# Optimization experiments

Measured on AMD Instinct MI355X. Metric: run time of the kernel, lower is better.

The kernel has to match this reference:

```python
import jax, jax.numpy as jnp
import numpy as np

QMIN, QMAX = 0, 255        # 8-bit asymmetric activation quant bounds
GROUP_SIZE = 128

def setup_inputs() -> dict:
    key = jax.random.key(0)
    k1, k2, k3, k4, k5 = jax.random.split(key, 5)
    x = jax.random.normal(k1, (1, 2048, 4096), dtype=jnp.float32)
    qweight = jax.random.randint(k2, (4096, 32, 128), 0, 16, dtype=jnp.int32)  # uint4 codes
    w_scales = jax.random.uniform(k3, (4096, 32), dtype=jnp.float32, minval=0.001, maxval=0.02)
    w_zero_points = jax.random.randint(k4, (4096, 32), 0, 16, dtype=jnp.int32)
    bias = jax.random.normal(k5, (4096,), dtype=jnp.float32)
    return {"x": x, "qweight": qweight, "w_scales": w_scales,
            "w_zero_points": w_zero_points, "bias": bias}

def reference(x, qweight, w_scales, w_zero_points, bias):
    xf = x.astype(jnp.float32)
    # per-token (last-dim) asymmetric dynamic activation quantization
    xmin = jnp.min(xf, axis=-1, keepdims=True)
    xmax = jnp.max(xf, axis=-1, keepdims=True)
    x_scale = jnp.clip((xmax - xmin) / (QMAX - QMIN), 1e-5, None)
    x_zp = jnp.clip(jnp.round(-xmin / x_scale), QMIN, QMAX)
    q = jnp.clip(jnp.round(xf / x_scale) + x_zp, QMIN, QMAX)
    centered_x = (q - x_zp).reshape(*x.shape[:-1], -1, GROUP_SIZE)  # [B,S,G,C]
    # grouped weight dequant (zero-point centered)
    centered_w = qweight.astype(jnp.float32) - w_zero_points.astype(jnp.float32)[..., None]  # [O,G,C]
    acc = jnp.einsum('bsgc,ogc->bsog', centered_x, centered_w)  # [B,S,O,G]
    out = (acc * w_scales[None, None]).sum(axis=-1)  # apply per-group weight scales
    out = out * x_scale  # per-token activation scale
    out = out + bias
    return out
```

## Files before the change

### kernel.cpp

```cpp
#include <hip/hip_runtime.h>
#include <stdint.h>

#define M_DIM 2048
#define N_DIM 4096
#define K_DIM 4096
#define NGROUP 32
#define GSIZE 128

#define RQ_UP   (127.0f / 15.0f)
#define RQ_DOWN (15.0f / 127.0f)

#define BM 256
#define BN 128
#define KSLICE 64
#define NSLICE (K_DIM / KSLICE)
#define BSLOT (BN * KSLICE)

typedef __attribute__((ext_vector_type(4))) int int32x4_t;

static __device__ __forceinline__ void gl2lds16(const void* g, void* l) {
    auto gp = (const __attribute__((address_space(1))) unsigned int*)(uintptr_t)g;
    auto lp = (__attribute__((address_space(3))) unsigned int*)(uintptr_t)l;
    __builtin_amdgcn_global_load_lds(gp, lp, 16, 0, 0);
}

#define WAITVM_(N) asm volatile("s_waitcnt vmcnt(" #N ")" ::: "memory")
#define WAITVM(N) WAITVM_(N)
#define WAITLGKM_(N) asm volatile("s_waitcnt lgkmcnt(" #N ")" ::: "memory")
#define WAITLGKM(N) WAITLGKM_(N)
#define BARRIER() asm volatile("s_barrier" ::: "memory")

#define QUANT_BLOCKS M_DIM
#define DEQ_BLOCKS ((N_DIM * K_DIM) / 8 / 256)

__global__ __launch_bounds__(256) void prep_kernel(
        const float* __restrict__ x,
        const int* __restrict__ qw,
        const float* __restrict__ wsc,
        const int* __restrict__ wzp,
        char* __restrict__ A8,
        char* __restrict__ Bt8,
        float* __restrict__ xscale,
        float* __restrict__ xzpc,
        int* __restrict__ Sw)
{
    const int t = threadIdx.x;
    if (blockIdx.x < QUANT_BLOCKS) {
        const int s = blockIdx.x;
        const float* xrow = x + (size_t)s * K_DIM;

        float xv[16];
        float vmin = 1e38f, vmax = -1e38f;
#pragma unroll
        for (int p = 0; p < 4; ++p) {
            float4 v = *((const float4*)(xrow + p * 1024) + t);
            xv[p*4+0] = v.x; xv[p*4+1] = v.y; xv[p*4+2] = v.z; xv[p*4+3] = v.w;
            vmin = fminf(vmin, fminf(fminf(v.x, v.y), fminf(v.z, v.w)));
            vmax = fmaxf(vmax, fmaxf(fmaxf(v.x, v.y), fmaxf(v.z, v.w)));
        }
#pragma unroll
        for (int off = 32; off > 0; off >>= 1) {
            vmin = fminf(vmin, __shfl_xor(vmin, off));
            vmax = fmaxf(vmax, __shfl_xor(vmax, off));
        }
        __shared__ float smin[4], smax[4];
        const int wave = t >> 6;
        if ((t & 63) == 0) { smin[wave] = vmin; smax[wave] = vmax; }
        __syncthreads();
        vmin = fminf(fminf(smin[0], smin[1]), fminf(smin[2], smin[3]));
        vmax = fmaxf(fmaxf(smax[0], smax[1]), fmaxf(smax[2], smax[3]));

        float sc = (vmax - vmin) / 255.0f;
        sc = fmaxf(sc, 1e-5f);
        float zp = rintf(-vmin / sc);
        zp = fminf(fmaxf(zp, 0.0f), 255.0f);

#pragma unroll
        for (int p = 0; p < 4; ++p) {
            int b[4];
#pragma unroll
            for (int e = 0; e < 4; ++e) {
                float q = fminf(fmaxf(rintf(xv[p*4+e] / sc) + zp, 0.0f), 255.0f);
                b[e] = (int)q - 128;
            }
            unsigned pack = (b[0] & 0xff) | ((b[1] & 0xff) << 8) |
                            ((b[2] & 0xff) << 16) | ((b[3] & 0xff) << 24);
            *(unsigned*)(A8 + (size_t)s * K_DIM + p * 1024 + t * 4) = pack;
        }
        if (t == 0) { xscale[s] = sc; xzpc[s] = 128.0f - zp; }
    } else {
        const size_t base = ((size_t)(blockIdx.x - QUANT_BLOCKS) * 256 + t) * 8;
        const int n = (int)(base >> 12);
        const int g = (int)((base >> 7) & 31);
        const int zp = wzp[n * NGROUP + g];

        const int cl = t & 15;
        float2 wp = *(const float2*)(wsc + (size_t)n * NGROUP + cl * 2);
        float smx = fmaxf(wp.x, wp.y);
#pragma unroll
        for (int off = 1; off < 16; off <<= 1)
            smx = fmaxf(smx, __shfl_xor(smx, off));
        const float factor = wsc[n * NGROUP + g] * (RQ_UP / smx);

        int4 c0 = *(const int4*)(qw + base);
        int4 c1 = *(const int4*)(qw + base + 4);
        int w[8];
        w[0] = (int)rintf((float)(c0.x - zp) * factor);
        w[1] = (int)rintf((float)(c0.y - zp) * factor);
        w[2] = (int)rintf((float)(c0.z - zp) * factor);
        w[3] = (int)rintf((float)(c0.w - zp) * factor);
        w[4] = (int)rintf((float)(c1.x - zp) * factor);
        w[5] = (int)rintf((float)(c1.y - zp) * factor);
        w[6] = (int)rintf((float)(c1.z - zp) * factor);
        w[7] = (int)rintf((float)(c1.w - zp) * factor);
        uint2 pk;
        pk.x = (w[0] & 0xff) | ((w[1] & 0xff) << 8) | ((w[2] & 0xff) << 16) | ((w[3] & 0xff) << 24);
        pk.y = (w[4] & 0xff) | ((w[5] & 0xff) << 8) | ((w[6] & 0xff) << 16) | ((w[7] & 0xff) << 24);
        *(uint2*)(Bt8 + base) = pk;

        int s8 = w[0] + w[1] + w[2] + w[3] + w[4] + w[5] + w[6] + w[7];
#pragma unroll
        for (int off = 1; off < 16; off <<= 1) s8 += __shfl_xor(s8, off);
        if ((t & 15) == 0)
            Sw[n * NGROUP + g] = s8;
    }
}

__global__ __launch_bounds__(512, 1) void gemm_kernel(
        const char* __restrict__ A8,
        const char* __restrict__ Bt8,
        const float* __restrict__ xscale,
        const float* __restrict__ xzpc,
        const float* __restrict__ wsc,
        const int* __restrict__ Sw,
        const float* __restrict__ bias,
        float* __restrict__ out)
{
    __shared__ __align__(16) char Bs[4][BSLOT];
    __shared__ float fws_s[BN], wsf_s[BN];

    const int tid  = threadIdx.x;
    const int bn   = blockIdx.x;
    const int bm   = blockIdx.y;
    const int wave = tid >> 6;
    const int lane = tid & 63;
    const int wr   = wave >> 1;
    const int wcl  = wave & 1;
    const int lrow  = lane & 15;
    const int lquad = lane >> 4;

    if (tid < BN) {
        const int n = bn * BN + tid;
        const int4* s4 = (const int4*)(Sw + (size_t)n * NGROUP);
        int acc = 0;
#pragma unroll
        for (int p = 0; p < 8; ++p) { int4 v = s4[p]; acc += v.x + v.y + v.z + v.w; }
        const float4* w4 = (const float4*)(wsc + (size_t)n * NGROUP);
        float s = 0.f;
#pragma unroll
        for (int p = 0; p < 8; ++p) {
            float4 w = w4[p];
            s = fmaxf(s, fmaxf(fmaxf(w.x, w.y), fmaxf(w.z, w.w)));
        }
        const float fw = s * RQ_DOWN;
        fws_s[tid] = fw;
        wsf_s[tid] = fw * (float)acc;
    }
    asm volatile("s_waitcnt vmcnt(0) lgkmcnt(0)" ::: "memory");

    const char* Bb = Bt8 + (size_t)(bn * BN) * K_DIM;
    const int lsub = lane >> 2;
    const int csrc = (lane & 3) ^ ((lane >> 3) & 3);
    const char* gB0 = Bb + (size_t)(wave * 16 + lsub) * K_DIM + csrc * 16;
    const int lB0 = wave * 1024;

    const char* gA = A8 + (size_t)(bm * BM + wr * 64 + lrow) * K_DIM + lquad * 16;

    const int xq = (lquad ^ ((lrow >> 1) & 3)) * 16;
    int boff[4];
#pragma unroll
    for (int j = 0; j < 4; ++j)
        boff[j] = (wcl * 64 + j * 16 + lrow) * KSLICE + xq;

    int32x4_t iacc[4][4];
    const int32x4_t zi = {0, 0, 0, 0};
#pragma unroll
    for (int i = 0; i < 4; ++i)
#pragma unroll
        for (int j = 0; j < 4; ++j) iacc[i][j] = zi;

    int32x4_t aX[4], aY[4], bX[4], bY[4];

#define STAGEB(t) gl2lds16(gB0 + (size_t)(t) * KSLICE, &Bs[(t) & 3][0] + lB0)

#define LOADA(t, ar) {                                                \
        _Pragma("unroll")                                             \
        for (int i_ = 0; i_ < 4; ++i_)                                \
            ar[i_] = *(const int32x4_t*)(gA + (size_t)i_ * 16 * K_DIM \
                                            + (size_t)(t) * KSLICE);  \
    }

#define READB(t, br) {                                                \
        const char* Bp_ = &Bs[(t) & 3][0];                            \
        _Pragma("unroll")                                             \
        for (int j_ = 0; j_ < 4; ++j_)                                \
            br[j_] = *(const int32x4_t*)(Bp_ + boff[j_]);             \
    }

#define MFMAS(ar, br) {                                               \
        __builtin_amdgcn_s_setprio(1);                                \
        _Pragma("unroll")                                             \
        for (int i_ = 0; i_ < 4; ++i_)                                \
            _Pragma("unroll")                                         \
            for (int j_ = 0; j_ < 4; ++j_)                            \
                iacc[i_][j_] = __builtin_amdgcn_mfma_i32_16x16x64_i8( \
                    ar[i_], br[j_], iacc[i_][j_], 0, 0, 0);           \
        __builtin_amdgcn_s_setprio(0);                                \
    }

#define BODY(s, VMN, AC, AN, BC, BNX) {                               \
        if ((s) + 3 < NSLICE) STAGEB((s) + 3);                        \
        WAITVM(VMN);                                                  \
        BARRIER();                                                    \
        READB((s) + 1, BNX);                                          \
        WAITLGKM(4);                                                  \
        __builtin_amdgcn_sched_barrier(0);                            \
        MFMAS(AC, BC);                                                \
        if ((s) + 2 < NSLICE) LOADA((s) + 2, AC);                     \
    }

    STAGEB(0); LOADA(0, aX);
    STAGEB(1); LOADA(1, aY);
    STAGEB(2);
    WAITVM(10);
    BARRIER();
    READB(0, bX);

    for (int s = 0; s < NSLICE - 4; s += 2) {
        BODY(s,     6, aX, aY, bX, bY);
        BODY(s + 1, 6, aY, aX, bY, bX);
    }
    BODY(60, 6, aX, aY, bX, bY);
    BODY(61, 5, aY, aX, bY, bX);
    WAITVM(4);
    BARRIER();
    READB(63, bY);
    WAITLGKM(4);
    __builtin_amdgcn_sched_barrier(0);
    MFMAS(aX, bX);
    WAITVM(0);
    WAITLGKM(0);
    __builtin_amdgcn_sched_barrier(0);
    MFMAS(aY, bY);

    float fn[4], wf[4], bb[4];
    int ncol[4];
#pragma unroll
    for (int j = 0; j < 4; ++j) {
        const int ncl = wcl * 64 + j * 16 + lrow;
        ncol[j] = bn * BN + ncl;
        fn[j] = fws_s[ncl];
        wf[j] = wsf_s[ncl];
        bb[j] = bias[ncol[j]];
    }
    const int m0 = bm * BM + wr * 64;
#pragma unroll
    for (int i = 0; i < 4; ++i) {
#pragma unroll
        for (int r = 0; r < 4; ++r) {
            const int m = m0 + i * 16 + lquad * 4 + r;
            const float xs  = xscale[m];
            const float czp = xzpc[m];
            float* orow = out + (size_t)m * N_DIM;
#pragma unroll
            for (int j = 0; j < 4; ++j)
                orow[ncol[j]] = xs * (fn[j] * (float)iacc[i][j][r] + czp * wf[j]) + bb[j];
        }
    }
#undef BODY
#undef MFMAS
#undef READB
#undef LOADA
#undef STAGEB
}

extern "C" void kernel_launch(void* const* d_in, const int* in_sizes, int n_in,
                              void* d_out, int out_size, void* d_ws, size_t ws_size,
                              hipStream_t stream) {
    const float* x     = (const float*)d_in[0];
    const int*   qw    = (const int*)d_in[1];
    const float* wsc   = (const float*)d_in[2];
    const int*   wzp   = (const int*)d_in[3];
    const float* bias  = (const float*)d_in[4];
    float* out = (float*)d_out;

    char* A8  = (char*)d_ws;
    char* Bt8 = A8 + (size_t)M_DIM * K_DIM;
    float* xscale = (float*)(Bt8 + (size_t)N_DIM * K_DIM);
    float* xzpc   = xscale + M_DIM;
    int*   Sw     = (int*)(xzpc + M_DIM);

    prep_kernel<<<QUANT_BLOCKS + DEQ_BLOCKS, 256, 0, stream>>>(
        x, qw, wsc, wzp, A8, Bt8, xscale, xzpc, Sw);
    dim3 grid(N_DIM / BN, M_DIM / BM);
    gemm_kernel<<<grid, 512, 0, stream>>>(A8, Bt8, xscale, xzpc, wsc, Sw, bias, out);
}
```

Before: 196.4 us.

## Shrink GEMM tile to 128x128 with 4 waves, stage A through LDS too

Moves from a 256x128 tile with 8 waves (A loaded directly from global into registers) to a 128x128 tile with 4 waves per block, two blocks per CU. Both A and B are now staged into a 4-slot LDS ring with global_load_lds, and fragments are read from swizzled LDS. The intent is better occupancy and latency hiding through two resident blocks, plus coalesced A loads. In exchange each block reuses less data, since A and B are fetched twice as often per output tile, and a second barrier is added per slice.

New measurement: 172.1 us. 12.4% less time.

```diff
diff --git a/kernel.cpp b/kernel.cpp
--- a/kernel.cpp
+++ b/kernel.cpp
@@ -10,10 +10,11 @@
 #define RQ_UP   (127.0f / 15.0f)
 #define RQ_DOWN (15.0f / 127.0f)
 
-#define BM 256
+#define BM 128
 #define BN 128
 #define KSLICE 64
 #define NSLICE (K_DIM / KSLICE)
+#define ASLOT (BM * KSLICE)
 #define BSLOT (BN * KSLICE)
 
 typedef __attribute__((ext_vector_type(4))) int int32x4_t;
@@ -126,7 +127,7 @@
     }
 }
 
-__global__ __launch_bounds__(512, 1) void gemm_kernel(
+__global__ __launch_bounds__(256, 2) void gemm_kernel(
         const char* __restrict__ A8,
         const char* __restrict__ Bt8,
         const float* __restrict__ xscale,
@@ -136,6 +137,7 @@
         const float* __restrict__ bias,
         float* __restrict__ out)
 {
+    __shared__ __align__(16) char As[4][ASLOT];
     __shared__ __align__(16) char Bs[4][BSLOT];
     __shared__ float fws_s[BN], wsf_s[BN];
 
@@ -168,16 +170,21 @@
     }
     asm volatile("s_waitcnt vmcnt(0) lgkmcnt(0)" ::: "memory");
 
+    const char* Ab = A8  + (size_t)(bm * BM) * K_DIM;
     const char* Bb = Bt8 + (size_t)(bn * BN) * K_DIM;
     const int lsub = lane >> 2;
     const int csrc = (lane & 3) ^ ((lane >> 3) & 3);
-    const char* gB0 = Bb + (size_t)(wave * 16 + lsub) * K_DIM + csrc * 16;
-    const int lB0 = wave * 1024;
-
-    const char* gA = A8 + (size_t)(bm * BM + wr * 64 + lrow) * K_DIM + lquad * 16;
+    const char* gA0 = Ab + (size_t)((wave * 16     ) + lsub) * K_DIM + csrc * 16;
+    const char* gA1 = Ab + (size_t)((wave * 16 + 64) + lsub) * K_DIM + csrc * 16;
+    const char* gB0 = Bb + (size_t)((wave * 16     ) + lsub) * K_DIM + csrc * 16;
+    const char* gB1 = Bb + (size_t)((wave * 16 + 64) + lsub) * K_DIM + csrc * 16;
+    const int lOF = wave * 1024;
 
     const int xq = (lquad ^ ((lrow >> 1) & 3)) * 16;
-    int boff[4];
+    int aoff[4], boff[4];
+#pragma unroll
+    for (int i = 0; i < 4; ++i)
+        aoff[i] = (wr * 64 + i * 16 + lrow) * KSLICE + xq;
 #pragma unroll
     for (int j = 0; j < 4; ++j)
         boff[j] = (wcl * 64 + j * 16 + lrow) * KSLICE + xq;
@@ -189,66 +196,67 @@
 #pragma unroll
         for (int j = 0; j < 4; ++j) iacc[i][j] = zi;
 
-    int32x4_t aX[4], aY[4], bX[4], bY[4];
-
-#define STAGEB(t) gl2lds16(gB0 + (size_t)(t) * KSLICE, &Bs[(t) & 3][0] + lB0)
-
-#define LOADA(t, ar) {                                                \
+    int32x4_t aX[4], bX[4], aY[4], bY[4];
+
+#define STAGE(t) {                                                    \
+        const int sl_ = (t) & 3;                                      \
+        const size_t k0_ = (size_t)(t) * KSLICE;                      \
+        gl2lds16(gA0 + k0_, &As[sl_][0] + lOF);                       \
+        gl2lds16(gA1 + k0_, &As[sl_][0] + 4096 + lOF);                \
+        gl2lds16(gB0 + k0_, &Bs[sl_][0] + lOF);                       \
+        gl2lds16(gB1 + k0_, &Bs[sl_][0] + 4096 + lOF);                \
+    }
+
+#define READF(t, af, bf) {                                            \
+        const char* Ap_ = &As[(t) & 3][0];                            \
+        const char* Bp_ = &Bs[(t) & 3][0];                            \
         _Pragma("unroll")                                             \
         for (int i_ = 0; i_ < 4; ++i_)                                \
-            ar[i_] = *(const int32x4_t*)(gA + (size_t)i_ * 16 * K_DIM \
-                                            + (size_t)(t) * KSLICE);  \
-    }
-
-#define READB(t, br) {                                                \
-        const char* Bp_ = &Bs[(t) & 3][0];                            \
+            af[i_] = *(const int32x4_t*)(Ap_ + aoff[i_]);             \
         _Pragma("unroll")                                             \
         for (int j_ = 0; j_ < 4; ++j_)                                \
-            br[j_] = *(const int32x4_t*)(Bp_ + boff[j_]);             \
-    }
-
-#define MFMAS(ar, br) {                                               \
+            bf[j_] = *(const int32x4_t*)(Bp_ + boff[j_]);             \
+    }
+
+#define MFMAS(af, bf) {                                               \
         __builtin_amdgcn_s_setprio(1);                                \
         _Pragma("unroll")                                             \
         for (int i_ = 0; i_ < 4; ++i_)                                \
             _Pragma("unroll")                                         \
             for (int j_ = 0; j_ < 4; ++j_)                            \
                 iacc[i_][j_] = __builtin_amdgcn_mfma_i32_16x16x64_i8( \
-                    ar[i_], br[j_], iacc[i_][j_], 0, 0, 0);           \
+                    af[i_], bf[j_], iacc[i_][j_], 0, 0, 0);           \
         __builtin_amdgcn_s_setprio(0);                                \
     }
 
-#define BODY(s, VMN, AC, AN, BC, BNX) {                               \
-        if ((s) + 3 < NSLICE) STAGEB((s) + 3);                        \
+#define BODY(s, VMN, CA, CB, NA, NB) {                                \
+        if ((s) + 3 < NSLICE) STAGE((s) + 3);                         \
         WAITVM(VMN);                                                  \
         BARRIER();                                                    \
-        READB((s) + 1, BNX);                                          \
-        WAITLGKM(4);                                                  \
+        READF((s) + 1, NA, NB);                                       \
+        WAITLGKM(8);                                                  \
         __builtin_amdgcn_sched_barrier(0);                            \
-        MFMAS(AC, BC);                                                \
-        if ((s) + 2 < NSLICE) LOADA((s) + 2, AC);                     \
-    }
-
-    STAGEB(0); LOADA(0, aX);
-    STAGEB(1); LOADA(1, aY);
-    STAGEB(2);
-    WAITVM(10);
+        MFMAS(CA, CB);                                                \
+        BARRIER();                                                    \
+    }
+
+    STAGE(0); STAGE(1); STAGE(2);
+    WAITVM(8);
     BARRIER();
-    READB(0, bX);
+    READF(0, aX, bX);
 
     for (int s = 0; s < NSLICE - 4; s += 2) {
-        BODY(s,     6, aX, aY, bX, bY);
-        BODY(s + 1, 6, aY, aX, bY, bX);
-    }
-    BODY(60, 6, aX, aY, bX, bY);
-    BODY(61, 5, aY, aX, bY, bX);
-    WAITVM(4);
+        BODY(s,     8, aX, bX, aY, bY);
+        BODY(s + 1, 8, aY, bY, aX, bX);
+    }
+    BODY(60, 8, aX, bX, aY, bY);
+    BODY(61, 4, aY, bY, aX, bX);
+    WAITVM(0);
     BARRIER();
-    READB(63, bY);
-    WAITLGKM(4);
+    READF(63, aY, bY);
+    WAITLGKM(8);
     __builtin_amdgcn_sched_barrier(0);
     MFMAS(aX, bX);
-    WAITVM(0);
     WAITLGKM(0);
     __builtin_amdgcn_sched_barrier(0);
     MFMAS(aY, bY);
@@ -279,9 +287,8 @@
     }
 #undef BODY
 #undef MFMAS
-#undef READB
-#undef LOADA
-#undef STAGEB
+#undef READF
+#undef STAGE
 }
 
 extern "C" void kernel_launch(void* const* d_in, const int* in_sizes, int n_in,
@@ -303,5 +310,5 @@
     prep_kernel<<<QUANT_BLOCKS + DEQ_BLOCKS, 256, 0, stream>>>(
         x, qw, wsc, wzp, A8, Bt8, xscale, xzpc, Sw);
     dim3 grid(N_DIM / BN, M_DIM / BM);
-    gemm_kernel<<<grid, 512, 0, stream>>>(A8, Bt8, xscale, xzpc, wsc, Sw, bias, out);
+    gemm_kernel<<<grid, 256, 0, stream>>>(A8, Bt8, xscale, xzpc, wsc, Sw, bias, out);
 }
```

## Pre-tile int8 operands into fragment layout and drop LDS staging in GEMM

Applied to the files above, without the earlier changes.

The prep kernel now writes quantized activations and weights in a tiled, pre-swizzled layout: 128 rows by 64 bytes per k-slice, stored contiguously. The GEMM loads MFMA fragments straight from global memory into registers, with no LDS, no barriers and no explicit waitcnt scheduling. It uses 256 threads with a 128x256 block tile, so each wave computes 64x128 with 4x8 accumulators. It also swaps a division for a reciprocal multiply in activation quantization. Dropping LDS reuse means each wave relies on L2/L1 for operand sharing, and the larger accumulator tile raises register pressure.

Result: faster. 173.0 us (-11.9%).

```diff
diff --git a/kernel.cpp b/kernel.cpp
--- a/kernel.cpp
+++ b/kernel.cpp
@@ -10,25 +10,11 @@
 #define RQ_UP   (127.0f / 15.0f)
 #define RQ_DOWN (15.0f / 127.0f)
 
-#define BM 256
-#define BN 128
-#define KSLICE 64
-#define NSLICE (K_DIM / KSLICE)
-#define BSLOT (BN * KSLICE)
+#define BM 128
+#define BN 256
+#define NSLICE (K_DIM / 64)
 
 typedef __attribute__((ext_vector_type(4))) int int32x4_t;
-
-static __device__ __forceinline__ void gl2lds16(const void* g, void* l) {
-    auto gp = (const __attribute__((address_space(1))) unsigned int*)(uintptr_t)g;
-    auto lp = (__attribute__((address_space(3))) unsigned int*)(uintptr_t)l;
-    __builtin_amdgcn_global_load_lds(gp, lp, 16, 0, 0);
-}
-
-#define WAITVM_(N) asm volatile("s_waitcnt vmcnt(" #N ")" ::: "memory")
-#define WAITVM(N) WAITVM_(N)
-#define WAITLGKM_(N) asm volatile("s_waitcnt lgkmcnt(" #N ")" ::: "memory")
-#define WAITLGKM(N) WAITLGKM_(N)
-#define BARRIER() asm volatile("s_barrier" ::: "memory")
 
 #define QUANT_BLOCKS M_DIM
 #define DEQ_BLOCKS ((N_DIM * K_DIM) / 8 / 256)
@@ -74,18 +60,25 @@
         sc = fmaxf(sc, 1e-5f);
         float zp = rintf(-vmin / sc);
         zp = fminf(fmaxf(zp, 0.0f), 255.0f);
-
+        const float inv_sc = 1.0f / sc;
+
+        const int r   = s & 127;
+        const int mt  = s >> 7;
+        const int swr = (r >> 1) & 3;
 #pragma unroll
         for (int p = 0; p < 4; ++p) {
             int b[4];
 #pragma unroll
             for (int e = 0; e < 4; ++e) {
-                float q = fminf(fmaxf(rintf(xv[p*4+e] / sc) + zp, 0.0f), 255.0f);
+                float q = fminf(fmaxf(rintf(xv[p*4+e] * inv_sc) + zp, 0.0f), 255.0f);
                 b[e] = (int)q - 128;
             }
             unsigned pack = (b[0] & 0xff) | ((b[1] & 0xff) << 8) |
                             ((b[2] & 0xff) << 16) | ((b[3] & 0xff) << 24);
-            *(unsigned*)(A8 + (size_t)s * K_DIM + p * 1024 + t * 4) = pack;
+            const int kt   = p * 16 + (t >> 4);
+            const int slot = ((t >> 2) & 3) ^ swr;
+            *(unsigned*)(A8 + (((size_t)(mt * 64 + kt)) << 13)
+                            + r * 64 + slot * 16 + (t & 3) * 4) = pack;
         }
         if (t == 0) { xscale[s] = sc; xzpc[s] = 128.0f - zp; }
     } else {
@@ -116,7 +109,13 @@
         uint2 pk;
         pk.x = (w[0] & 0xff) | ((w[1] & 0xff) << 8) | ((w[2] & 0xff) << 16) | ((w[3] & 0xff) << 24);
         pk.y = (w[4] & 0xff) | ((w[5] & 0xff) << 8) | ((w[6] & 0xff) << 16) | ((w[7] & 0xff) << 24);
-        *(uint2*)(Bt8 + base) = pk;
+
+        const int r  = n & 127;
+        const int nt = n >> 7;
+        const int kt = (int)((base >> 6) & 63);
+        const int slot = (int)(((base >> 4) & 3)) ^ ((r >> 1) & 3);
+        *(uint2*)(Bt8 + (((size_t)(nt * 64 + kt)) << 13)
+                      + r * 64 + slot * 16 + (int)(base & 15)) = pk;
 
         int s8 = w[0] + w[1] + w[2] + w[3] + w[4] + w[5] + w[6] + w[7];
 #pragma unroll
@@ -126,7 +125,7 @@
     }
 }
 
-__global__ __launch_bounds__(512, 1) void gemm_kernel(
+__global__ __launch_bounds__(256, 1) void gemm_kernel(
         const char* __restrict__ A8,
         const char* __restrict__ Bt8,
         const float* __restrict__ xscale,
@@ -136,7 +135,6 @@
         const float* __restrict__ bias,
         float* __restrict__ out)
 {
-    __shared__ __align__(16) char Bs[4][BSLOT];
     __shared__ float fws_s[BN], wsf_s[BN];
 
     const int tid  = threadIdx.x;
@@ -149,7 +147,7 @@
     const int lrow  = lane & 15;
     const int lquad = lane >> 4;
 
-    if (tid < BN) {
+    {
         const int n = bn * BN + tid;
         const int4* s4 = (const int4*)(Sw + (size_t)n * NGROUP);
         int acc = 0;
@@ -166,98 +164,61 @@
         fws_s[tid] = fw;
         wsf_s[tid] = fw * (float)acc;
     }
-    asm volatile("s_waitcnt vmcnt(0) lgkmcnt(0)" ::: "memory");
-
-    const char* Bb = Bt8 + (size_t)(bn * BN) * K_DIM;
-    const int lsub = lane >> 2;
-    const int csrc = (lane & 3) ^ ((lane >> 3) & 3);
-    const char* gB0 = Bb + (size_t)(wave * 16 + lsub) * K_DIM + csrc * 16;
-    const int lB0 = wave * 1024;
-
-    const char* gA = A8 + (size_t)(bm * BM + wr * 64 + lrow) * K_DIM + lquad * 16;
 
     const int xq = (lquad ^ ((lrow >> 1) & 3)) * 16;
-    int boff[4];
-#pragma unroll
-    for (int j = 0; j < 4; ++j)
-        boff[j] = (wcl * 64 + j * 16 + lrow) * KSLICE + xq;
-
-    int32x4_t iacc[4][4];
+    const char* pA = A8 + ((size_t)bm << 19)
+                        + (size_t)(wr * 64 + lrow) * 64 + xq;
+    const char* pB = Bt8 + ((size_t)(bn * 2 + wcl) << 19)
+                        + (size_t)lrow * 64 + xq;
+
+    int32x4_t iacc[4][8];
     const int32x4_t zi = {0, 0, 0, 0};
 #pragma unroll
     for (int i = 0; i < 4; ++i)
 #pragma unroll
-        for (int j = 0; j < 4; ++j) iacc[i][j] = zi;
-
-    int32x4_t aX[4], aY[4], bX[4], bY[4];
-
-#define STAGEB(t) gl2lds16(gB0 + (size_t)(t) * KSLICE, &Bs[(t) & 3][0] + lB0)
-
-#define LOADA(t, ar) {                                                \
+        for (int j = 0; j < 8; ++j) iacc[i][j] = zi;
+
+#define LOADF(s, aF, bF) {                                            \
+        const char* a_ = pA + ((size_t)(s) << 13);                    \
+        const char* b_ = pB + ((size_t)(s) << 13);                    \
         _Pragma("unroll")                                             \
         for (int i_ = 0; i_ < 4; ++i_)                                \
-            ar[i_] = *(const int32x4_t*)(gA + (size_t)i_ * 16 * K_DIM \
-                                            + (size_t)(t) * KSLICE);  \
-    }
-
-#define READB(t, br) {                                                \
-        const char* Bp_ = &Bs[(t) & 3][0];                            \
+            aF[i_] = *(const int32x4_t*)(a_ + i_ * 1024);             \
         _Pragma("unroll")                                             \
-        for (int j_ = 0; j_ < 4; ++j_)                                \
-            br[j_] = *(const int32x4_t*)(Bp_ + boff[j_]);             \
-    }
-
-#define MFMAS(ar, br) {                                               \
-        __builtin_amdgcn_s_setprio(1);                                \
+        for (int j_ = 0; j_ < 8; ++j_)                                \
+            bF[j_] = *(const int32x4_t*)(b_ + j_ * 1024);             \
+    }
+
+#define MFMAS(aF, bF) {                                               \
         _Pragma("unroll")                                             \
         for (int i_ = 0; i_ < 4; ++i_)                                \
             _Pragma("unroll")                                         \
-            for (int j_ = 0; j_ < 4; ++j_)                            \
+            for (int j_ = 0; j_ < 8; ++j_)                            \
                 iacc[i_][j_] = __builtin_amdgcn_mfma_i32_16x16x64_i8( \
-                    ar[i_], br[j_], iacc[i_][j_], 0, 0, 0);           \
-        __builtin_amdgcn_s_setprio(0);                                \
-    }
-
-#define BODY(s, VMN, AC, AN, BC, BNX) {                               \
-        if ((s) + 3 < NSLICE) STAGEB((s) + 3);                        \
-        WAITVM(VMN);                                                  \
-        BARRIER();                                                    \
-        READB((s) + 1, BNX);                                          \
-        WAITLGKM(4);                                                  \
-        __builtin_amdgcn_sched_barrier(0);                            \
-        MFMAS(AC, BC);                                                \
-        if ((s) + 2 < NSLICE) LOADA((s) + 2, AC);                     \
-    }
-
-    STAGEB(0); LOADA(0, aX);
-    STAGEB(1); LOADA(1, aY);
-    STAGEB(2);
-    WAITVM(10);
-    BARRIER();
-    READB(0, bX);
-
-    for (int s = 0; s < NSLICE - 4; s += 2) {
-        BODY(s,     6, aX, aY, bX, bY);
-        BODY(s + 1, 6, aY, aX, bY, bX);
-    }
-    BODY(60, 6, aX, aY, bX, bY);
-    BODY(61, 5, aY, aX, bY, bX);
-    WAITVM(4);
-    BARRIER();
-    READB(63, bY);
-    WAITLGKM(4);
-    __builtin_amdgcn_sched_barrier(0);
+                    aF[i_], bF[j_], iacc[i_][j_], 0, 0, 0);           \
+    }
+
+    int32x4_t aX[4], bX[8], aY[4], bY[8];
+
+    LOADF(0, aX, bX);
+    LOADF(1, aY, bY);
+#pragma unroll 1
+    for (int s = 0; s < NSLICE - 2; s += 2) {
+        MFMAS(aX, bX);
+        LOADF(s + 2, aX, bX);
+        MFMAS(aY, bY);
+        LOADF(s + 3, aY, bY);
+    }
     MFMAS(aX, bX);
-    WAITVM(0);
-    WAITLGKM(0);
-    __builtin_amdgcn_sched_barrier(0);
     MFMAS(aY, bY);
 
-    float fn[4], wf[4], bb[4];
-    int ncol[4];
-#pragma unroll
-    for (int j = 0; j < 4; ++j) {
-        const int ncl = wcl * 64 + j * 16 + lrow;
+    __syncthreads();
+
+    float fn[8], wf[8], bb[8];
+    int ncol[8];
+#pragma unroll
+    for (int j = 0; j < 8; ++j) {
+        const int ncl = wcl * 128 + j * 16 + lrow;
         ncol[j] = bn * BN + ncl;
         fn[j] = fws_s[ncl];
         wf[j] = wsf_s[ncl];
@@ -273,15 +234,12 @@
             const float czp = xzpc[m];
             float* orow = out + (size_t)m * N_DIM;
 #pragma unroll
-            for (int j = 0; j < 4; ++j)
+            for (int j = 0; j < 8; ++j)
                 orow[ncol[j]] = xs * (fn[j] * (float)iacc[i][j][r] + czp * wf[j]) + bb[j];
         }
     }
-#undef BODY
 #undef MFMAS
-#undef READB
-#undef LOADA
-#undef STAGEB
+#undef LOADF
 }
 
 extern "C" void kernel_launch(void* const* d_in, const int* in_sizes, int n_in,
@@ -302,6 +260,8 @@
 
     prep_kernel<<<QUANT_BLOCKS + DEQ_BLOCKS, 256, 0, stream>>>(
         x, qw, wsc, wzp, A8, Bt8, xscale, xzpc, Sw);
+
     dim3 grid(N_DIM / BN, M_DIM / BM);
-    gemm_kernel<<<grid, 512, 0, stream>>>(A8, Bt8, xscale, xzpc, wsc, Sw, bias, out);
+    gemm_kernel<<<grid, 256, 0, stream>>>(
+        A8, Bt8, xscale, xzpc, wsc, Sw, bias, out);
 }
```
